# Optimization experiments

Hardware: AMD Instinct MI355X
Metric: run time of the kernel (lower is better)

## Reference

```python
import jax, jax.numpy as jnp
import numpy as np

M = 8192          # flattened tokens (batch*seq)
IN_FEATURES = 4096
OUT_FEATURES = 4096


def setup_inputs() -> dict:
    key = jax.random.key(0)
    k1, k2, k3 = jax.random.split(key, 3)
    # int8-valued activations and weights, stored as int32 (values in [-128, 127])
    x = jax.random.randint(k1, (M, IN_FEATURES), -128, 128, dtype=jnp.int32)
    int_weight = jax.random.randint(k2, (OUT_FEATURES, IN_FEATURES), -128, 127, dtype=jnp.int32)
    bias = (jax.random.normal(k3, (OUT_FEATURES,), dtype=jnp.float32) * 0.02).astype(jnp.float16)
    return {"x": x, "int_weight": int_weight, "bias": bias}


def reference(x, int_weight, bias):
    # x.to(torch.int8); quik int8Matmul: int8 GEMM with int32 accumulation, out = x @ W^T
    x_i8 = x.astype(jnp.int8)
    w_i8 = int_weight.astype(jnp.int8)
    acc = jax.lax.dot_general(
        x_i8, w_i8,
        dimension_numbers=(((1,), (1,)), ((), ())),  # [M, K] x [N, K] -> [M, N]
        preferred_element_type=jnp.int32,
    )
    # .to(torch.float16) then bias add (fused epilogue target)
    return acc.astype(jnp.float16) + bias
```

## Files before the change

kernel.cpp:

```cpp
#include <hip/hip_runtime.h>

#define MDIM 8192
#define NDIM 4096
#define KDIM 4096
#define BM 256
#define BN 256
#define BK 128

typedef int v4i __attribute__((ext_vector_type(4)));
typedef int v16i __attribute__((ext_vector_type(16)));

__device__ __forceinline__ unsigned pack4(int x, int y, int z, int w) {
    return (unsigned)(x & 0xff) | ((unsigned)(y & 0xff) << 8) |
           ((unsigned)(z & 0xff) << 16) | ((unsigned)w << 24);
}

__global__ __launch_bounds__(256) void pack_tiled(const int* __restrict__ x,
                                                  const int* __restrict__ w,
                                                  uint4* __restrict__ xp,
                                                  uint4* __restrict__ wp) {
    __shared__ unsigned lds32[256 * 33];
    const int wg  = blockIdx.x;
    const int tid = threadIdx.x;
    const int kq   = tid & 31;
    const int rsub = tid >> 5;

    const int* src;
    uint4* dst;
    if (wg < 1024) {
        const int mtile = wg >> 5, kiter = wg & 31;
        src = x + (size_t)(mtile * 256) * KDIM + kiter * 128;
        dst = xp + (size_t)(mtile * 32 + kiter) * 2048;
    } else {
        const int ntile = (wg - 1024) >> 5, kiter = wg & 31;
        src = w + (size_t)(ntile * 256) * KDIM + kiter * 128;
        dst = wp + (size_t)(ntile * 32 + kiter) * 2048;
    }
#pragma unroll
    for (int it = 0; it < 32; ++it) {
        const int row = it * 8 + rsub;
        int4 v = *(const int4*)(src + (size_t)row * KDIM + kq * 4);
        lds32[row * 33 + kq] = pack4(v.x, v.y, v.z, v.w);
    }
    __syncthreads();
#pragma unroll
    for (int it = 0; it < 8; ++it) {
        const int g = it * 256 + tid;
        const int kb = g >> 8, row = g & 255;
        const unsigned* p = &lds32[row * 33 + kb * 4];
        uint4 o;
        o.x = p[0]; o.y = p[1]; o.z = p[2]; o.w = p[3];
        dst[g] = o;
    }
}

__global__ __launch_bounds__(512, 2) void gemm_i8_breg(const char* __restrict__ Ap,
                                                       const char* __restrict__ Bp,
                                                       const _Float16* __restrict__ bias,
                                                       _Float16* __restrict__ out) {
    __shared__ __align__(16) char lds[65536];

    const int tid  = threadIdx.x;
    const int lane = tid & 63;
    const int wave = tid >> 6;
    const int wr   = wave >> 2;
    const int wcn  = wave & 3;
    const int l31  = lane & 31;
    const int kg   = lane >> 5;

    const int lid = blockIdx.y * 16 + blockIdx.x;
    const int xc  = lid & 7, ii = lid >> 3;
    const int bx  = (xc & 3) * 4 + (ii & 3);
    const int by  = (xc >> 2) * 16 + (ii >> 2);
    const int bm0 = by * BM;
    const int bn0 = bx * BN;

    const char* apan = Ap + (size_t)by * (BM * KDIM) + tid * 16;
    const char* bpan = Bp + (size_t)bx * (BN * KDIM);

    int aoff[4], boffG[2];
#pragma unroll
    for (int mt = 0; mt < 4; ++mt)
        aoff[mt] = (wr * 128 + mt * 32 + l31) * 16 + kg * 4096;
#pragma unroll
    for (int nt = 0; nt < 2; ++nt)
        boffG[nt] = (wcn * 64 + nt * 32 + l31) * 16 + kg * 4096;

    v16i acc[4][2];
#pragma unroll
    for (int mt = 0; mt < 4; ++mt)
#pragma unroll
        for (int nt = 0; nt < 2; ++nt)
#pragma unroll
            for (int i = 0; i < 16; ++i) acc[mt][nt][i] = 0;

    v4i afP[4], afQ[4];
    v4i bfX[2][4], bfY[2][4];

    auto stageA = [&](int nb) {
#pragma unroll
        for (int c2 = 0; c2 < 4; ++c2)
            __builtin_amdgcn_global_load_lds(
                (__attribute__((address_space(1))) const void*)(apan + c2 * 8192),
                (__attribute__((address_space(3))) void*)(lds + nb + c2 * 8192 + tid * 16),
                16, 0, 0);
    };
    auto loadB = [&](v4i (&d)[2][4]) {
#pragma unroll
        for (int nt = 0; nt < 2; ++nt)
#pragma unroll
            for (int ks = 0; ks < 4; ++ks)
                d[nt][ks] = *(const v4i*)(bpan + boffG[nt] + ks * 8192);
    };
    auto readA = [&](v4i (&d)[4], int base, int ks) {
#pragma unroll
        for (int mt = 0; mt < 4; ++mt)
            d[mt] = *(const v4i*)(lds + base + ks * 8192 + aoff[mt]);
    };
    auto cl = [&](const v4i (&a)[4], const v4i (&b)[2][4], int k) {
        __builtin_amdgcn_s_setprio(1);
#pragma unroll
        for (int mt = 0; mt < 4; ++mt)
#pragma unroll
            for (int nt = 0; nt < 2; ++nt)
                acc[mt][nt] = __builtin_amdgcn_mfma_i32_32x32x32_i8(
                    a[mt], b[nt][k], acc[mt][nt], 0, 0, 0);
        __builtin_amdgcn_s_setprio(0);
    };

#define SB0 __builtin_amdgcn_sched_barrier(0)
#define TOPBAR do { asm volatile("s_waitcnt vmcnt(0)" ::: "memory"); \
                    __builtin_amdgcn_s_barrier(); } while (0)

    auto body = [&](int cur, const v4i (&bf)[2][4], int nxt, v4i (&bfn)[2][4],
                    bool stg) {
        TOPBAR; SB0;
        readA(afP, cur, 0);
        readA(afQ, cur, 1);
        SB0;
        if (stg) {
            stageA(nxt);
            loadB(bfn);
            apan += BM * BK;
            bpan += BN * BK;
        }
        SB0;
        cl(afP, bf, 0); SB0;
        readA(afP, cur, 2); SB0;
        cl(afQ, bf, 1); SB0;
        readA(afQ, cur, 3); SB0;
        cl(afP, bf, 2); SB0;
        cl(afQ, bf, 3);
    };

    stageA(0);
    loadB(bfX);
    apan += BM * BK;
    bpan += BN * BK;

    body(0, bfX, 32768, bfY, true);

#pragma unroll 1
    for (int p = 0; p < 15; ++p) {
        body(32768, bfY, 0, bfX, true);
        body(0, bfX, 32768, bfY, true);
    }
    body(32768, bfY, 0, bfX, false);

#undef SB0
#undef TOPBAR

    const _Float16 bv0 = bias[bn0 + wcn * 64 + l31];
    const _Float16 bv1 = bias[bn0 + wcn * 64 + 32 + l31];
#pragma unroll
    for (int mt = 0; mt < 4; ++mt) {
#pragma unroll
        for (int nt = 0; nt < 2; ++nt) {
            const int gcol = bn0 + wcn * 64 + nt * 32 + l31;
            const _Float16 bb = nt ? bv1 : bv0;
#pragma unroll
            for (int r = 0; r < 16; ++r) {
                const int rit  = (r & 3) + 8 * (r >> 2) + 4 * kg;
                const int grow = bm0 + wr * 128 + mt * 32 + rit;
                _Float16 h = (_Float16)(float)acc[mt][nt][r] + bb;
                out[(size_t)grow * NDIM + gcol] = h;
            }
        }
    }
}

__global__ __launch_bounds__(256, 2) void gemm_i8_fb(const int* __restrict__ A32,
                                                     const int* __restrict__ B32,
                                                     const _Float16* __restrict__ bias,
                                                     _Float16* __restrict__ out) {
    __shared__ char lds[32768];
    const int tid  = threadIdx.x;
    const int lane = tid & 63;
    const int wave = tid >> 6;
    const int bm0 = blockIdx.y * 256;
    const int bn0 = blockIdx.x * 128;
    const int wr  = wave >> 1;
    const int wc  = wave & 1;
    const int l31 = lane & 31;
    const int kg  = lane >> 5;

    int abase[4];
#pragma unroll
    for (int mt = 0; mt < 4; ++mt)
        abase[mt] = kg * 4096 + (wr * 128 + mt * 32 + l31) * 16;

    v16i acc[4][2];
#pragma unroll
    for (int mt = 0; mt < 4; ++mt)
#pragma unroll
        for (int nt = 0; nt < 2; ++nt)
#pragma unroll
            for (int i = 0; i < 16; ++i) acc[mt][nt][i] = 0;

    int aoffs[8];
#pragma unroll
    for (int r = 0; r < 8; ++r) {
        const int c = r * 4 + wave;
        aoffs[r] = (bm0 + (c & 3) * 64 + lane) * KDIM + (c >> 2) * 16;
    }
    for (int k0 = 0; k0 < KDIM; k0 += 128) {
        v4i bfx[2][4];
#pragma unroll
        for (int r = 0; r < 8; ++r) {
            const int c = r * 4 + wave;
            const int4* s = (const int4*)(A32 + (size_t)aoffs[r]);
            int4 v0 = s[0], v1 = s[1], v2 = s[2], v3 = s[3];
            uint4 pk;
            pk.x = pack4(v0.x, v0.y, v0.z, v0.w);
            pk.y = pack4(v1.x, v1.y, v1.z, v1.w);
            pk.z = pack4(v2.x, v2.y, v2.z, v2.w);
            pk.w = pack4(v3.x, v3.y, v3.z, v3.w);
            *(uint4*)(lds + c * 1024 + lane * 16) = pk;
            aoffs[r] += 128;
        }
#pragma unroll
        for (int nt = 0; nt < 2; ++nt)
#pragma unroll
            for (int ks = 0; ks < 4; ++ks) {
                const int* s = B32 + (size_t)(bn0 + wc * 64 + nt * 32 + l31) * KDIM
                               + k0 + (2 * ks + kg) * 16;
                int4 v0 = ((const int4*)s)[0], v1 = ((const int4*)s)[1];
                int4 v2 = ((const int4*)s)[2], v3 = ((const int4*)s)[3];
                bfx[nt][ks][0] = (int)pack4(v0.x, v0.y, v0.z, v0.w);
                bfx[nt][ks][1] = (int)pack4(v1.x, v1.y, v1.z, v1.w);
                bfx[nt][ks][2] = (int)pack4(v2.x, v2.y, v2.z, v2.w);
                bfx[nt][ks][3] = (int)pack4(v3.x, v3.y, v3.z, v3.w);
            }
        __syncthreads();
#pragma unroll
        for (int ks = 0; ks < 4; ++ks) {
            v4i afr[4];
#pragma unroll
            for (int mt = 0; mt < 4; ++mt)
                afr[mt] = *(const v4i*)(lds + abase[mt] + ks * 8192);
#pragma unroll
            for (int mt = 0; mt < 4; ++mt)
#pragma unroll
                for (int nt = 0; nt < 2; ++nt)
                    acc[mt][nt] = __builtin_amdgcn_mfma_i32_32x32x32_i8(
                        afr[mt], bfx[nt][ks], acc[mt][nt], 0, 0, 0);
        }
        __syncthreads();
    }

    const _Float16 bv0 = bias[bn0 + wc * 64 + l31];
    const _Float16 bv1 = bias[bn0 + wc * 64 + 32 + l31];
#pragma unroll
    for (int mt = 0; mt < 4; ++mt) {
#pragma unroll
        for (int nt = 0; nt < 2; ++nt) {
            const int gcol = bn0 + wc * 64 + nt * 32 + l31;
            const _Float16 bb = nt ? bv1 : bv0;
#pragma unroll
            for (int r = 0; r < 16; ++r) {
                const int rit  = (r & 3) + 8 * (r >> 2) + 4 * kg;
                const int grow = bm0 + wr * 128 + mt * 32 + rit;
                _Float16 h = (_Float16)(float)acc[mt][nt][r] + bb;
                out[(size_t)grow * NDIM + gcol] = h;
            }
        }
    }
}

extern "C" void kernel_launch(void* const* d_in, const int* in_sizes, int n_in,
                              void* d_out, int out_size, void* d_ws, size_t ws_size,
                              hipStream_t stream) {
    const int* x = (const int*)d_in[0];
    const int* w = (const int*)d_in[1];
    const _Float16* bias = (const _Float16*)d_in[2];
    _Float16* out = (_Float16*)d_out;

    const size_t xbytes = (size_t)MDIM * KDIM;
    const size_t wbytes = (size_t)NDIM * KDIM;

    if (ws_size >= xbytes + wbytes) {
        char* xp = (char*)d_ws;
        char* wp = xp + xbytes;
        pack_tiled<<<1536, 256, 0, stream>>>(x, w, (uint4*)xp, (uint4*)wp);
        gemm_i8_breg<<<dim3(NDIM / BN, MDIM / BM), 512, 0, stream>>>(
            (const char*)xp, (const char*)wp, bias, out);
    } else {
        gemm_i8_fb<<<dim3(NDIM / 128, MDIM / 256), 256, 0, stream>>>(
            x, w, bias, out);
    }
}
```

Before: 386.0 us.

## Replace 256x256 register-B GEMM with 128x128 tile, 4-block occupancy kernel

Replaces the 512-thread, 256x256-tile int8 GEMM, which kept B fragments in registers loaded straight from global memory, with a 256-thread, 128x128-tile kernel. The new kernel stages both A and B into double-buffered LDS through global_load_lds, reads B back from LDS, and targets four resident blocks per CU. It also remaps the XCD block swizzle for the 32x64 grid. The aim is to hide latency through more waves per CU instead of explicit register prefetch, at the cost of less data reuse per tile, more LDS traffic for B, and a barrier on every K step.

```diff
diff --git a/kernel.cpp b/kernel.cpp
--- a/kernel.cpp
+++ b/kernel.cpp
@@ -3,9 +3,6 @@
 #define MDIM 8192
 #define NDIM 4096
 #define KDIM 4096
-#define BM 256
-#define BN 256
-#define BK 128
 
 typedef int v4i __attribute__((ext_vector_type(4)));
 typedef int v16i __attribute__((ext_vector_type(16)));
@@ -54,77 +51,86 @@
     }
 }
 
-__global__ __launch_bounds__(512, 2) void gemm_i8_breg(const char* __restrict__ Ap,
-                                                       const char* __restrict__ Bp,
-                                                       const _Float16* __restrict__ bias,
-                                                       _Float16* __restrict__ out) {
-    __shared__ __align__(16) char lds[65536];
+__global__ __launch_bounds__(256, 4) void gemm_i8_tlp(const char* __restrict__ Ap,
+                                                      const char* __restrict__ Bp,
+                                                      const _Float16* __restrict__ bias,
+                                                      _Float16* __restrict__ out) {
+    __shared__ __align__(16) char lds[32768];
 
     const int tid  = threadIdx.x;
     const int lane = tid & 63;
     const int wave = tid >> 6;
-    const int wr   = wave >> 2;
-    const int wcn  = wave & 3;
+    const int wr   = wave >> 1;
+    const int wc   = wave & 1;
     const int l31  = lane & 31;
     const int kg   = lane >> 5;
 
-    const int lid = blockIdx.y * 16 + blockIdx.x;
-    const int xc  = lid & 7, ii = lid >> 3;
-    const int bx  = (xc & 3) * 4 + (ii & 3);
-    const int by  = (xc >> 2) * 16 + (ii >> 2);
-    const int bm0 = by * BM;
-    const int bn0 = bx * BN;
-
-    const char* apan = Ap + (size_t)by * (BM * KDIM) + tid * 16;
-    const char* bpan = Bp + (size_t)bx * (BN * KDIM);
-
-    int aoff[4], boffG[2];
-#pragma unroll
-    for (int mt = 0; mt < 4; ++mt)
-        aoff[mt] = (wr * 128 + mt * 32 + l31) * 16 + kg * 4096;
+    const int lid = blockIdx.y * 32 + blockIdx.x;
+    const int xcd = lid & 7, ii = lid >> 3;
+    const int bx  = (xcd & 1) * 16 + (ii & 15);
+    const int by  = (xcd >> 1) * 16 + (ii >> 4);
+    const int bm0 = by * 128;
+    const int bn0 = bx * 128;
+
+    const char* apan = Ap + (size_t)(by >> 1) * 1048576
+                     + (((tid >> 7) * 256) + (by & 1) * 128 + (tid & 127)) * 16;
+    const char* bpan = Bp + (size_t)(bx >> 1) * 1048576
+                     + (((tid >> 7) * 256) + (bx & 1) * 128 + (tid & 127)) * 16;
+
+    int aoffr[2], boffr[2];
+#pragma unroll
+    for (int mt = 0; mt < 2; ++mt)
+        aoffr[mt] = (wr * 64 + mt * 32 + l31) * 16;
 #pragma unroll
     for (int nt = 0; nt < 2; ++nt)
-        boffG[nt] = (wcn * 64 + nt * 32 + l31) * 16 + kg * 4096;
-
-    v16i acc[4][2];
-#pragma unroll
-    for (int mt = 0; mt < 4; ++mt)
+        boffr[nt] = 8192 + (wc * 64 + nt * 32 + l31) * 16;
+
+    v16i acc[2][2];
+#pragma unroll
+    for (int mt = 0; mt < 2; ++mt)
 #pragma unroll
         for (int nt = 0; nt < 2; ++nt)
 #pragma unroll
             for (int i = 0; i < 16; ++i) acc[mt][nt][i] = 0;
 
-    v4i afP[4], afQ[4];
-    v4i bfX[2][4], bfY[2][4];
-
-    auto stageA = [&](int nb) {
-#pragma unroll
-        for (int c2 = 0; c2 < 4; ++c2)
+    v4i afP[2], afQ[2], bf[2][2];
+
+    auto stage = [&](int nb) {
+#pragma unroll
+        for (int c = 0; c < 2; ++c)
             __builtin_amdgcn_global_load_lds(
-                (__attribute__((address_space(1))) const void*)(apan + c2 * 8192),
-                (__attribute__((address_space(3))) void*)(lds + nb + c2 * 8192 + tid * 16),
+                (__attribute__((address_space(1))) const void*)(apan + c * 8192),
+                (__attribute__((address_space(3))) void*)(lds + nb + c * 4096 + tid * 16),
                 16, 0, 0);
+#pragma unroll
+        for (int c = 0; c < 2; ++c)
+            __builtin_amdgcn_global_load_lds(
+                (__attribute__((address_space(1))) const void*)(bpan + c * 8192),
+                (__attribute__((address_space(3))) void*)(lds + nb + 8192 + c * 4096 + tid * 16),
+                16, 0, 0);
+        apan += 16384;
+        bpan += 16384;
     };
-    auto loadB = [&](v4i (&d)[2][4]) {
+    auto readA = [&](v4i (&d)[2], int base, int ks) {
+#pragma unroll
+        for (int mt = 0; mt < 2; ++mt)
+            d[mt] = *(const v4i*)(lds + base + (2 * ks + kg) * 2048 + aoffr[mt]);
+    };
+    auto readB = [&](int base) {
 #pragma unroll
         for (int nt = 0; nt < 2; ++nt)
 #pragma unroll
-            for (int ks = 0; ks < 4; ++ks)
-                d[nt][ks] = *(const v4i*)(bpan + boffG[nt] + ks * 8192);
+            for (int ks = 0; ks < 2; ++ks)
+                bf[nt][ks] = *(const v4i*)(lds + base + (2 * ks + kg) * 2048 + boffr[nt]);
     };
-    auto readA = [&](v4i (&d)[4], int base, int ks) {
-#pragma unroll
-        for (int mt = 0; mt < 4; ++mt)
-            d[mt] = *(const v4i*)(lds + base + ks * 8192 + aoff[mt]);
-    };
-    auto cl = [&](const v4i (&a)[4], const v4i (&b)[2][4], int k) {
+    auto cl = [&](const v4i (&a)[2], int k) {
         __builtin_amdgcn_s_setprio(1);
 #pragma unroll
-        for (int mt = 0; mt < 4; ++mt)
+        for (int mt = 0; mt < 2; ++mt)
 #pragma unroll
             for (int nt = 0; nt < 2; ++nt)
                 acc[mt][nt] = __builtin_amdgcn_mfma_i32_32x32x32_i8(
-                    a[mt], b[nt][k], acc[mt][nt], 0, 0, 0);
+                    a[mt], bf[nt][k], acc[mt][nt], 0, 0, 0);
         __builtin_amdgcn_s_setprio(0);
     };
 
@@ -132,56 +138,39 @@
 #define TOPBAR do { asm volatile("s_waitcnt vmcnt(0)" ::: "memory"); \
                     __builtin_amdgcn_s_barrier(); } while (0)
 
-    auto body = [&](int cur, const v4i (&bf)[2][4], int nxt, v4i (&bfn)[2][4],
-                    bool stg) {
-        TOPBAR; SB0;
+    stage(0);
+    TOPBAR; SB0;
+
+#pragma unroll 1
+    for (int t = 0; t < 64; ++t) {
+        const int cur = (t & 1) ? 16384 : 0;
+        if (t < 63) stage(cur ^ 16384);
+        readB(cur);
         readA(afP, cur, 0);
+        SB0;
         readA(afQ, cur, 1);
         SB0;
-        if (stg) {
-            stageA(nxt);
-            loadB(bfn);
-            apan += BM * BK;
-            bpan += BN * BK;
-        }
+        cl(afP, 0);
         SB0;
-        cl(afP, bf, 0); SB0;
-        readA(afP, cur, 2); SB0;
-        cl(afQ, bf, 1); SB0;
-        readA(afQ, cur, 3); SB0;
-        cl(afP, bf, 2); SB0;
-        cl(afQ, bf, 3);
-    };
-
-    stageA(0);
-    loadB(bfX);
-    apan += BM * BK;
-    bpan += BN * BK;
-
-    body(0, bfX, 32768, bfY, true);
-
-#pragma unroll 1
-    for (int p = 0; p < 15; ++p) {
-        body(32768, bfY, 0, bfX, true);
-        body(0, bfX, 32768, bfY, true);
-    }
-    body(32768, bfY, 0, bfX, false);
+        cl(afQ, 1);
+        if (t < 63) { TOPBAR; }
+    }
 
 #undef SB0
 #undef TOPBAR
 
-    const _Float16 bv0 = bias[bn0 + wcn * 64 + l31];
-    const _Float16 bv1 = bias[bn0 + wcn * 64 + 32 + l31];
-#pragma unroll
-    for (int mt = 0; mt < 4; ++mt) {
+    const _Float16 bv0 = bias[bn0 + wc * 64 + l31];
+    const _Float16 bv1 = bias[bn0 + wc * 64 + 32 + l31];
+#pragma unroll
+    for (int mt = 0; mt < 2; ++mt) {
 #pragma unroll
         for (int nt = 0; nt < 2; ++nt) {
-            const int gcol = bn0 + wcn * 64 + nt * 32 + l31;
+            const int gcol = bn0 + wc * 64 + nt * 32 + l31;
             const _Float16 bb = nt ? bv1 : bv0;
 #pragma unroll
             for (int r = 0; r < 16; ++r) {
                 const int rit  = (r & 3) + 8 * (r >> 2) + 4 * kg;
-                const int grow = bm0 + wr * 128 + mt * 32 + rit;
+                const int grow = bm0 + wr * 64 + mt * 32 + rit;
                 _Float16 h = (_Float16)(float)acc[mt][nt][r] + bb;
                 out[(size_t)grow * NDIM + gcol] = h;
             }
@@ -302,7 +291,7 @@
         char* xp = (char*)d_ws;
         char* wp = xp + xbytes;
         pack_tiled<<<1536, 256, 0, stream>>>(x, w, (uint4*)xp, (uint4*)wp);
-        gemm_i8_breg<<<dim3(NDIM / BN, MDIM / BM), 512, 0, stream>>>(
+        gemm_i8_tlp<<<dim3(32, 64), 256, 0, stream>>>(
             (const char*)xp, (const char*)wp, bias, out);
     } else {
         gemm_i8_fb<<<dim3(NDIM / 128, MDIM / 256), 256, 0, stream>>>(
```

New measurement: 407.7 us. +5.6%, slower.
